# Performance work log

Hardware: AMD Instinct MI355X
Metric: run time of the kernel (lower is better)

The kernel has to match this reference:

```python
import jax, jax.numpy as jnp
import numpy as np

B, N, C, H = 2, 2048, 1024, 16
D = C // H  # head_dim = 64


def _rope_freqs(n, d_half, theta=10000.0):
    inv = 1.0 / (theta ** (np.arange(0, d_half, dtype=np.float32) / d_half))
    ang = np.arange(n, dtype=np.float32)[:, None] * inv[None, :]
    return jnp.asarray(np.cos(ang)), jnp.asarray(np.sin(ang))


def setup_inputs() -> dict:
    key = jax.random.key(0)
    ks = jax.random.split(key, 5)
    cos, sin = _rope_freqs(N, D // 2)
    s = 0.02
    return {
        "x": jax.random.normal(ks[0], (B, N, C), jnp.float32),
        "w_qkv": jax.random.normal(ks[1], (3 * C, C), jnp.float32) * s,
        "b_qkv": jnp.zeros((3 * C,), jnp.float32),
        "w_proj": jax.random.normal(ks[2], (C, C), jnp.float32) * s,
        "b_proj": jnp.zeros((C,), jnp.float32),
        "freqs_cos": cos,
        "freqs_sin": sin,
    }


def _apply_rope(t, cos, sin):
    # t: (B, H, N, D); consecutive pairs (even, odd) form complex numbers,
    # matching torch.view_as_complex on reshape(..., D//2, 2).
    te = t[..., 0::2]
    to = t[..., 1::2]
    cos = cos[None, None, :, :]  # (1,1,N,D//2)
    sin = sin[None, None, :, :]
    oe = te * cos - to * sin
    oo = te * sin + to * cos
    return jnp.stack([oe, oo], axis=-1).reshape(t.shape)


def reference(x, w_qkv, b_qkv, w_proj, b_proj, freqs_cos, freqs_sin):
    b, n, c = x.shape
    qkv = x @ w_qkv.T + b_qkv                      # (B,N,3C)
    qkv = qkv.reshape(b, n, 3, H, D).transpose(2, 0, 3, 1, 4)  # (3,B,H,N,D)
    q, k, v = qkv[0], qkv[1], qkv[2]
    q = _apply_rope(q, freqs_cos, freqs_sin)
    k = _apply_rope(k, freqs_cos, freqs_sin)
    scale = 1.0 / jnp.sqrt(jnp.asarray(D, x.dtype))
    scores = jnp.einsum("bhqd,bhkd->bhqk", q, k) * scale
    attn = jax.nn.softmax(scores, axis=-1)
    out = jnp.einsum("bhqk,bhkd->bhqd", attn, v)   # (B,H,N,D)
    out = out.transpose(0, 2, 1, 3).reshape(b, n, c)
    return out @ w_proj.T + b_proj
```

## Files before the change

kernel.cpp:

```cpp
#include <hip/hip_runtime.h>
#include <hip/hip_bf16.h>
#include <stdint.h>

#define BB 2
#define NN 2048
#define CC 1024
#define HH 16
#define DD 64
#define C3 3072

typedef __attribute__((ext_vector_type(8))) short bf16x8;
typedef __attribute__((ext_vector_type(4))) short bf16x4;
typedef __attribute__((ext_vector_type(4))) float f32x4;
typedef __attribute__((ext_vector_type(4))) unsigned short ushort4_t;

__device__ __forceinline__ unsigned short f2bf(float f) {
  union { float f; unsigned u; } v; v.f = f;
  unsigned r = v.u + 0x7FFFu + ((v.u >> 16) & 1u);
  return (unsigned short)(r >> 16);
}

#if __has_builtin(__builtin_amdgcn_exp2f)
#define EXP2(x) __builtin_amdgcn_exp2f(x)
#else
#define EXP2(x) exp2f(x)
#endif

#if __has_builtin(__builtin_amdgcn_mfma_f32_16x16x16bf16_1k)
#define HAVE_MFMA16 1
#endif

__device__ __forceinline__ unsigned pack_bf2(float a, float b) {
  union { float f; unsigned u; } ua, ub; ua.f = a; ub.f = b;
#if __has_builtin(__builtin_amdgcn_perm)
  return __builtin_amdgcn_perm(ub.u, ua.u, 0x07060302u);
#else
  return (ua.u >> 16) | (ub.u & 0xFFFF0000u);
#endif
}

#define QSCALE 0.18033688f

#define GLDS(g, l) __builtin_amdgcn_global_load_lds( \
    (const __attribute__((address_space(1))) void*)(g), \
    (__attribute__((address_space(3))) void*)(l), 16, 0, 0)

__global__ __launch_bounds__(256) void k_cvt(
    const float* __restrict__ x, const float* __restrict__ wq,
    const float* __restrict__ wp,
    unsigned short* __restrict__ xb, unsigned short* __restrict__ wqb,
    unsigned short* __restrict__ wpb)
{
  int blk = blockIdx.x;
  const float* s; unsigned short* d; int i;
  if (blk < 4096)      { s = x;  d = xb;  i = blk * 256 + threadIdx.x; }
  else if (blk < 7168) { s = wq; d = wqb; i = (blk - 4096) * 256 + threadIdx.x; }
  else                 { s = wp; d = wpb; i = (blk - 7168) * 256 + threadIdx.x; }
  float4 v = ((const float4*)s)[i];
  ushort4_t o;
  o.x = f2bf(v.x); o.y = f2bf(v.y); o.z = f2bf(v.z); o.w = f2bf(v.w);
  ((ushort4_t*)d)[i] = o;
}

__global__ __launch_bounds__(256) void k_gemm_qkv(
    const unsigned short* __restrict__ A, const unsigned short* __restrict__ Bt,
    const float* __restrict__ bias,
    const float* __restrict__ cosb, const float* __restrict__ sinb,
    unsigned short* __restrict__ Qg, unsigned short* __restrict__ Kg,
    unsigned short* __restrict__ Vt)
{
  __shared__ __align__(16) unsigned short Sh[16384];
  const int tid  = threadIdx.x;
  const int lane = tid & 63;
  const int wave = tid >> 6;
  const int bm = blockIdx.y * 128;
  const int bn = blockIdx.x * 128;
  const int wm = (wave >> 1) * 64;
  const int wn = (wave & 1) * 64;
  const int frow = lane & 15;
  const int fk   = (lane >> 4) * 8;
  const int K = 1024;
  const int NIT = K / 32;

  f32x4 acc[4][4] = {};

  const int row0 = tid >> 2, cc0 = tid & 3;
  const int row1 = row0 + 64;
  const unsigned short* Arow0 = A  + (size_t)(bm + row0) * K + cc0 * 8;
  const unsigned short* Arow1 = A  + (size_t)(bm + row1) * K + cc0 * 8;
  const unsigned short* Brow0 = Bt + (size_t)(bn + row0) * K + cc0 * 8;
  const unsigned short* Brow1 = Bt + (size_t)(bn + row1) * K + cc0 * 8;

  GLDS(Arow0, Sh + (size_t)tid * 8);
  GLDS(Brow0, Sh + 4096 + (size_t)tid * 8);
  GLDS(Arow1, Sh + (size_t)(tid + 256) * 8);
  GLDS(Brow1, Sh + 4096 + (size_t)(tid + 256) * 8);

  for (int it = 0; it < NIT; ++it) {
    const int p = it & 1;
    const unsigned short* As = Sh + p * 8192;
    const unsigned short* Bs = As + 4096;
    __syncthreads();

    if (it + 1 < NIT) {
      const int k1 = (it + 1) * 32;
      unsigned short* An = Sh + (1 - p) * 8192;
      GLDS(Arow0 + k1, An + (size_t)tid * 8);
      GLDS(Brow0 + k1, An + 4096 + (size_t)tid * 8);
      GLDS(Arow1 + k1, An + (size_t)(tid + 256) * 8);
      GLDS(Brow1 + k1, An + 4096 + (size_t)(tid + 256) * 8);
    }

    bf16x8 af[4], bfr[4];
#pragma unroll
    for (int t = 0; t < 4; ++t) {
      af[t]  = *(const bf16x8*)(As + (wm + t * 16 + frow) * 32 + fk);
      bfr[t] = *(const bf16x8*)(Bs + (wn + t * 16 + frow) * 32 + fk);
    }
#pragma unroll
    for (int mt = 0; mt < 4; ++mt)
#pragma unroll
      for (int nt = 0; nt < 4; ++nt)
        acc[mt][nt] = __builtin_amdgcn_mfma_f32_16x16x32_bf16(af[mt], bfr[nt], acc[mt][nt], 0, 0, 0);
  }
  __syncthreads();

  const int er0  = (lane >> 4) * 4;
  const int ecol = lane & 15;
  const int region = bn >> 10;
  const int gcol0 = bn + wn;
  const int h  = (gcol0 >> 6) & 15;
  const int rowg0 = bm + wm;
  const int b  = rowg0 >> 11;
  const int n0 = rowg0 & (NN - 1);
  unsigned short* wt = Sh + wave * 4096;

#pragma unroll
  for (int nt = 0; nt < 4; ++nt) {
    const int c64 = nt * 16 + ecol;
    const float bv = bias[gcol0 + c64];
    const int ii  = c64 >> 1;
#pragma unroll
    for (int mt = 0; mt < 4; ++mt)
#pragma unroll
      for (int r = 0; r < 4; ++r) {
        const int ml = mt * 16 + er0 + r;
        const int n  = n0 + ml;
        float v = acc[mt][nt][r] + bv;
        float vp = __shfl_xor(v, 1, 64);
        if (region == 2) {
          wt[c64 * 64 + ((((ml >> 3) ^ (c64 & 7)) << 3) | (ml & 7))] = f2bf(v);
        } else {
          float cth = cosb[n * 32 + ii], sth = sinb[n * 32 + ii];
          float ov = (c64 & 1) ? (vp * sth + v * cth)
                               : (v * cth - vp * sth);
          if (region == 0) ov *= QSCALE;
          wt[ml * 64 + ((((c64 >> 3) ^ (ml & 7)) << 3) | (c64 & 7))] = f2bf(ov);
        }
      }
  }

  const int rr = lane >> 3, cc = lane & 7;
  if (region == 2) {
    unsigned short* dst = Vt + (size_t)(b * HH + h) * DD * NN + n0;
#pragma unroll
    for (int it = 0; it < 8; ++it) {
      int dl = it * 8 + rr;
      bf16x8 vv = *(const bf16x8*)(wt + dl * 64 + ((cc ^ (dl & 7)) << 3));
      *(bf16x8*)(dst + (size_t)dl * NN + cc * 8) = vv;
    }
  } else {
    unsigned short* dqk = ((region == 0) ? Qg : Kg) +
                          ((size_t)(b * HH + h) * NN + n0) * DD;
#pragma unroll
    for (int it = 0; it < 8; ++it) {
      int ml = it * 8 + rr;
      bf16x8 vv = *(const bf16x8*)(wt + ml * 64 + ((cc ^ (ml & 7)) << 3));
      *(bf16x8*)(dqk + (size_t)ml * DD + cc * 8) = vv;
    }
  }
}

__global__ __launch_bounds__(256) void k_attn(
    const unsigned short* __restrict__ Qg, const unsigned short* __restrict__ Kg,
    const unsigned short* __restrict__ Vtg, unsigned short* __restrict__ Og)
{
  __shared__ __align__(16) unsigned short Ks[2][64 * 64];
  __shared__ __align__(16) unsigned short Vs[2][64 * 64];
#ifndef HAVE_MFMA16
  __shared__ __align__(16) unsigned short Ps[4][32 * 64];
#endif

  const int tid  = threadIdx.x;
  const int lane = tid & 63;
  const int wave = tid >> 6;
  const int bh = blockIdx.x >> 4;
  const int qt = blockIdx.x & 15;
  const int q0 = qt * 128 + wave * 32;
  const int frow   = lane & 15;
  const int fchunk = lane >> 4;
  const int er0  = (lane >> 4) * 4;
  const int ecol = lane & 15;

  const unsigned short* Qb = Qg  + (size_t)bh * NN * DD;
  const unsigned short* Kb = Kg  + (size_t)bh * NN * DD;
  const unsigned short* Vb = Vtg + (size_t)bh * DD * NN;

  bf16x8 qf[2][2];
#pragma unroll
  for (int m = 0; m < 2; ++m)
#pragma unroll
    for (int kt = 0; kt < 2; ++kt)
      qf[m][kt] = *(const bf16x8*)(Qb + (size_t)(q0 + m * 16 + frow) * DD + kt * 32 + fchunk * 8);

  f32x4 oacc[2][4] = {};

  const int row0 = tid >> 3, cc0 = tid & 7;
  const int sw0 = (cc0 ^ (row0 & 7)) * 8;

  GLDS(Kb + (size_t)row0 * DD + sw0,        Ks[0] + (size_t)tid * 8);
  GLDS(Vb + (size_t)row0 * NN + sw0,        Vs[0] + (size_t)tid * 8);
  GLDS(Kb + (size_t)(row0 + 32) * DD + sw0, Ks[0] + (size_t)(tid + 256) * 8);
  GLDS(Vb + (size_t)(row0 + 32) * NN + sw0, Vs[0] + (size_t)(tid + 256) * 8);

#ifdef HAVE_MFMA16
  float lsum[2] = {0.f, 0.f};

  for (int t = 0; t < NN / 64; ++t) {
    const int p = t & 1;
    __syncthreads();

    if (t + 1 < NN / 64) {
      const int j = (t + 1) * 64;
      GLDS(Kb + (size_t)(j + row0) * DD + sw0,      Ks[1 - p] + (size_t)tid * 8);
      GLDS(Vb + (size_t)row0 * NN + j + sw0,        Vs[1 - p] + (size_t)tid * 8);
      GLDS(Kb + (size_t)(j + row0 + 32) * DD + sw0, Ks[1 - p] + (size_t)(tid + 256) * 8);
      GLDS(Vb + (size_t)(row0 + 32) * NN + j + sw0, Vs[1 - p] + (size_t)(tid + 256) * 8);
    }

    f32x4 sacc[2][4] = {};
#pragma unroll
    for (int nt = 0; nt < 4; ++nt) {
      int kr = nt * 16 + frow;
      bf16x8 kf0 = *(const bf16x8*)(Ks[p] + kr * 64 + ((fchunk       ^ (kr & 7)) << 3));
      bf16x8 kf1 = *(const bf16x8*)(Ks[p] + kr * 64 + (((fchunk + 4) ^ (kr & 7)) << 3));
#pragma unroll
      for (int m = 0; m < 2; ++m) {
        sacc[m][nt] = __builtin_amdgcn_mfma_f32_16x16x32_bf16(kf0, qf[m][0], sacc[m][nt], 0, 0, 0);
        sacc[m][nt] = __builtin_amdgcn_mfma_f32_16x16x32_bf16(kf1, qf[m][1], sacc[m][nt], 0, 0, 0);
      }
    }

    bf16x4 pfr[2][4];
#pragma unroll
    for (int m = 0; m < 2; ++m)
#pragma unroll
      for (int nt = 0; nt < 4; ++nt) {
        float e0 = EXP2(sacc[m][nt][0]);
        float e1 = EXP2(sacc[m][nt][1]);
        float e2 = EXP2(sacc[m][nt][2]);
        float e3 = EXP2(sacc[m][nt][3]);
        lsum[m] += (e0 + e1) + (e2 + e3);
        union { unsigned u[2]; bf16x4 v; } pk;
        pk.u[0] = pack_bf2(e0, e1);
        pk.u[1] = pack_bf2(e2, e3);
        pfr[m][nt] = pk.v;
      }

#pragma unroll
    for (int dt = 0; dt < 4; ++dt) {
      int vr = dt * 16 + frow;
      bf16x4 vfr[4];
#pragma unroll
      for (int c = 0; c < 4; ++c)
        vfr[c] = *(const bf16x4*)(Vs[p] + vr * 64 +
                   (((2 * c + (fchunk >> 1)) ^ (vr & 7)) << 3) + (fchunk & 1) * 4);
#pragma unroll
      for (int m = 0; m < 2; ++m)
#pragma unroll
        for (int c = 0; c < 4; ++c)
          oacc[m][dt] = __builtin_amdgcn_mfma_f32_16x16x16bf16_1k(pfr[m][c], vfr[c], oacc[m][dt], 0, 0, 0);
    }
  }

  const int b = bh >> 4;
  const int h = bh & 15;
#pragma unroll
  for (int m = 0; m < 2; ++m) {
    lsum[m] += __shfl_xor(lsum[m], 16, 64);
    lsum[m] += __shfl_xor(lsum[m], 32, 64);
    float linv[4];
#pragma unroll
    for (int r = 0; r < 4; ++r)
      linv[r] = 1.0f / __shfl(lsum[m], er0 + r, 64);
#pragma unroll
    for (int dt = 0; dt < 4; ++dt)
#pragma unroll
      for (int r = 0; r < 4; ++r) {
        int qrow = q0 + m * 16 + er0 + r;
        int d = dt * 16 + ecol;
        Og[(size_t)(b * NN + qrow) * CC + h * DD + d] = f2bf(oacc[m][dt][r] * linv[r]);
      }
  }

#else
  bf16x8 ones;
#pragma unroll
  for (int i = 0; i < 8; ++i) ones[i] = (short)0x3F80;
  f32x4 lacc[2] = {};

  for (int t = 0; t < NN / 64; ++t) {
    const int p = t & 1;
    __syncthreads();
    if (t + 1 < NN / 64) {
      const int j = (t + 1) * 64;
      GLDS(Kb + (size_t)(j + row0) * DD + sw0,      Ks[1 - p] + (size_t)tid * 8);
      GLDS(Vb + (size_t)row0 * NN + j + sw0,        Vs[1 - p] + (size_t)tid * 8);
      GLDS(Kb + (size_t)(j + row0 + 32) * DD + sw0, Ks[1 - p] + (size_t)(tid + 256) * 8);
      GLDS(Vb + (size_t)(row0 + 32) * NN + j + sw0, Vs[1 - p] + (size_t)(tid + 256) * 8);
    }
    f32x4 sacc[2][4] = {};
#pragma unroll
    for (int nt = 0; nt < 4; ++nt) {
      int kr = nt * 16 + frow;
      bf16x8 kf0 = *(const bf16x8*)(Ks[p] + kr * 64 + ((fchunk       ^ (kr & 7)) << 3));
      bf16x8 kf1 = *(const bf16x8*)(Ks[p] + kr * 64 + (((fchunk + 4) ^ (kr & 7)) << 3));
#pragma unroll
      for (int m = 0; m < 2; ++m) {
        sacc[m][nt] = __builtin_amdgcn_mfma_f32_16x16x32_bf16(qf[m][0], kf0, sacc[m][nt], 0, 0, 0);
        sacc[m][nt] = __builtin_amdgcn_mfma_f32_16x16x32_bf16(qf[m][1], kf1, sacc[m][nt], 0, 0, 0);
      }
    }
#pragma unroll
    for (int m = 0; m < 2; ++m)
#pragma unroll
      for (int r = 0; r < 4; ++r) {
        int prow = m * 16 + er0 + r;
#pragma unroll
        for (int nt = 0; nt < 4; ++nt) {
          float pv = EXP2(sacc[m][nt][r]);
          union { float f; unsigned u; } cv; cv.f = pv;
          int col = nt * 16 + ecol;
          Ps[wave][prow * 64 + (((col >> 3) ^ (prow & 7)) << 3) + (col & 7)] =
              (unsigned short)(cv.u >> 16);
        }
      }
    bf16x8 pf0[2], pf1[2];
#pragma unroll
    for (int m = 0; m < 2; ++m) {
      int pr = m * 16 + frow;
      pf0[m] = *(const bf16x8*)(&Ps[wave][pr * 64 + ((fchunk       ^ (pr & 7)) << 3)]);
      pf1[m] = *(const bf16x8*)(&Ps[wave][pr * 64 + (((fchunk + 4) ^ (pr & 7)) << 3)]);
      lacc[m] = __builtin_amdgcn_mfma_f32_16x16x32_bf16(pf0[m], ones, lacc[m], 0, 0, 0);
      lacc[m] = __builtin_amdgcn_mfma_f32_16x16x32_bf16(pf1[m], ones, lacc[m], 0, 0, 0);
    }
#pragma unroll
    for (int dt = 0; dt < 4; ++dt) {
      int vr = dt * 16 + frow;
      bf16x8 vf0 = *(const bf16x8*)(Vs[p] + vr * 64 + ((fchunk       ^ (vr & 7)) << 3));
      bf16x8 vf1 = *(const bf16x8*)(Vs[p] + vr * 64 + (((fchunk + 4) ^ (vr & 7)) << 3));
#pragma unroll
      for (int m = 0; m < 2; ++m) {
        oacc[m][dt] = __builtin_amdgcn_mfma_f32_16x16x32_bf16(pf0[m], vf0, oacc[m][dt], 0, 0, 0);
        oacc[m][dt] = __builtin_amdgcn_mfma_f32_16x16x32_bf16(pf1[m], vf1, oacc[m][dt], 0, 0, 0);
      }
    }
  }
  const int b = bh >> 4;
  const int h = bh & 15;
#pragma unroll
  for (int m = 0; m < 2; ++m)
#pragma unroll
    for (int dt = 0; dt < 4; ++dt)
#pragma unroll
      for (int r = 0; r < 4; ++r) {
        int qrow = q0 + m * 16 + er0 + r;
        int d = dt * 16 + ecol;
        Og[(size_t)(b * NN + qrow) * CC + h * DD + d] = f2bf(oacc[m][dt][r] / lacc[m][r]);
      }
#endif
}

__global__ __launch_bounds__(256) void k_gemm_proj(
    const unsigned short* __restrict__ A, const unsigned short* __restrict__ Bt,
    const float* __restrict__ bias, float* __restrict__ Co)
{
  __shared__ __align__(16) unsigned short As[2][64 * 32];
  __shared__ __align__(16) unsigned short Bs[2][128 * 32];
  const int tid  = threadIdx.x;
  const int lane = tid & 63;
  const int wave = tid >> 6;
  const int bm = blockIdx.y * 64;
  const int bn = blockIdx.x * 128;
  const int wm = (wave >> 1) * 32;
  const int wn = (wave & 1) * 64;
  const int frow = lane & 15;
  const int fk   = (lane >> 4) * 8;
  const int K = 1024;
  const int NIT = K / 32;

  f32x4 acc[2][4] = {};

  const int row0 = tid >> 2, cc0 = tid & 3;
  const unsigned short* Arow  = A  + (size_t)(bm + row0) * K + cc0 * 8;
  const unsigned short* Brow0 = Bt + (size_t)(bn + row0) * K + cc0 * 8;
  const unsigned short* Brow1 = Bt + (size_t)(bn + row0 + 64) * K + cc0 * 8;

  GLDS(Arow,  As[0] + (size_t)tid * 8);
  GLDS(Brow0, Bs[0] + (size_t)tid * 8);
  GLDS(Brow1, Bs[0] + (size_t)(tid + 256) * 8);

  for (int it = 0; it < NIT; ++it) {
    const int p = it & 1;
    __syncthreads();

    if (it + 1 < NIT) {
      const int k1 = (it + 1) * 32;
      GLDS(Arow  + k1, As[1 - p] + (size_t)tid * 8);
      GLDS(Brow0 + k1, Bs[1 - p] + (size_t)tid * 8);
      GLDS(Brow1 + k1, Bs[1 - p] + (size_t)(tid + 256) * 8);
    }

    bf16x8 af[2], bfr[4];
#pragma unroll
    for (int t = 0; t < 2; ++t)
      af[t] = *(const bf16x8*)(As[p] + (wm + t * 16 + frow) * 32 + fk);
#pragma unroll
    for (int t = 0; t < 4; ++t)
      bfr[t] = *(const bf16x8*)(Bs[p] + (wn + t * 16 + frow) * 32 + fk);
#pragma unroll
    for (int mt = 0; mt < 2; ++mt)
#pragma unroll
      for (int nt = 0; nt < 4; ++nt)
        acc[mt][nt] = __builtin_amdgcn_mfma_f32_16x16x32_bf16(af[mt], bfr[nt], acc[mt][nt], 0, 0, 0);
  }

  const int er0  = (lane >> 4) * 4;
  const int ecol = lane & 15;
#pragma unroll
  for (int nt = 0; nt < 4; ++nt) {
    int col = bn + wn + nt * 16 + ecol;
    float bv = bias[col];
#pragma unroll
    for (int mt = 0; mt < 2; ++mt)
#pragma unroll
      for (int r = 0; r < 4; ++r) {
        int rowg = bm + wm + mt * 16 + er0 + r;
        Co[(size_t)rowg * CC + col] = acc[mt][nt][r] + bv;
      }
  }
}

extern "C" void kernel_launch(void* const* d_in, const int* in_sizes, int n_in,
                              void* d_out, int out_size, void* d_ws, size_t ws_size,
                              hipStream_t stream)
{
  const float* x      = (const float*)d_in[0];
  const float* w_qkv  = (const float*)d_in[1];
  const float* b_qkv  = (const float*)d_in[2];
  const float* w_proj = (const float*)d_in[3];
  const float* b_proj = (const float*)d_in[4];
  const float* fcos   = (const float*)d_in[5];
  const float* fsin   = (const float*)d_in[6];
  float* out = (float*)d_out;

  char* ws = (char*)d_ws;
  unsigned short* xb     = (unsigned short*)(ws);
  unsigned short* wqkvb  = (unsigned short*)(ws + 8388608);
  unsigned short* wprojb = (unsigned short*)(ws + 14680064);
  unsigned short* Qb     = (unsigned short*)(ws + 16777216);
  unsigned short* Kb     = (unsigned short*)(ws + 25165824);
  unsigned short* Vtb    = (unsigned short*)(ws + 33554432);
  unsigned short* aob    = (unsigned short*)(ws + 41943040);

  k_cvt<<<8192, 256, 0, stream>>>(x, w_qkv, w_proj, xb, wqkvb, wprojb);

  k_gemm_qkv<<<dim3(24, 32), 256, 0, stream>>>(xb, wqkvb, b_qkv, fcos, fsin,
                                               Qb, Kb, Vtb);

  k_attn<<<512, 256, 0, stream>>>(Qb, Kb, Vtb, aob);

  k_gemm_proj<<<dim3(8, 64), 256, 0, stream>>>(aob, wprojb, b_proj, out);
}
```

Before: 215.5 us.

## Switch attention kernel to 32x32x16 MFMA tiles with transposed score layout

Rewrites the attention inner loop to use 32x32x16 bf16 MFMA for both QK^T and PV instead of 16x16 variants, computing transposed scores so the exponentiated probabilities feed the PV MFMA directly from registers. LDS offsets are precomputed per lane, and the row sum reduces across two half-waves only. This aims to cut MFMA instruction count and LDS fragment loads per tile, at the cost of larger accumulator register footprint and a different output write pattern. The non-MFMA16 fallback path is removed.

```diff
diff --git a/kernel.cpp b/kernel.cpp
--- a/kernel.cpp
+++ b/kernel.cpp
@@ -12,6 +12,7 @@
 typedef __attribute__((ext_vector_type(8))) short bf16x8;
 typedef __attribute__((ext_vector_type(4))) short bf16x4;
 typedef __attribute__((ext_vector_type(4))) float f32x4;
+typedef __attribute__((ext_vector_type(16))) float f32x16;
 typedef __attribute__((ext_vector_type(4))) unsigned short ushort4_t;
 
 __device__ __forceinline__ unsigned short f2bf(float f) {
@@ -24,10 +25,6 @@
 #define EXP2(x) __builtin_amdgcn_exp2f(x)
 #else
 #define EXP2(x) exp2f(x)
-#endif
-
-#if __has_builtin(__builtin_amdgcn_mfma_f32_16x16x16bf16_1k)
-#define HAVE_MFMA16 1
 #endif
 
 __device__ __forceinline__ unsigned pack_bf2(float a, float b) {
@@ -187,9 +184,6 @@
 {
   __shared__ __align__(16) unsigned short Ks[2][64 * 64];
   __shared__ __align__(16) unsigned short Vs[2][64 * 64];
-#ifndef HAVE_MFMA16
-  __shared__ __align__(16) unsigned short Ps[4][32 * 64];
-#endif
 
   const int tid  = threadIdx.x;
   const int lane = tid & 63;
@@ -197,23 +191,31 @@
   const int bh = blockIdx.x >> 4;
   const int qt = blockIdx.x & 15;
   const int q0 = qt * 128 + wave * 32;
-  const int frow   = lane & 15;
-  const int fchunk = lane >> 4;
-  const int er0  = (lane >> 4) * 4;
-  const int ecol = lane & 15;
+  const int l31 = lane & 31;
+  const int hi  = lane >> 5;
+  const int s7  = l31 & 7;
 
   const unsigned short* Qb = Qg  + (size_t)bh * NN * DD;
   const unsigned short* Kb = Kg  + (size_t)bh * NN * DD;
   const unsigned short* Vb = Vtg + (size_t)bh * DD * NN;
 
-  bf16x8 qf[2][2];
-#pragma unroll
-  for (int m = 0; m < 2; ++m)
-#pragma unroll
-    for (int kt = 0; kt < 2; ++kt)
-      qf[m][kt] = *(const bf16x8*)(Qb + (size_t)(q0 + m * 16 + frow) * DD + kt * 32 + fchunk * 8);
-
-  f32x4 oacc[2][4] = {};
+  int koff[4];
+#pragma unroll
+  for (int x = 0; x < 4; ++x)
+    koff[x] = l31 * 64 + (((2 * x + hi) ^ s7) << 3);
+
+  int vkoff[8];
+#pragma unroll
+  for (int c = 0; c < 8; ++c)
+    vkoff[c] = l31 * 64 + ((c ^ s7) << 3) + hi * 4;
+
+  bf16x8 qf[4];
+#pragma unroll
+  for (int dc = 0; dc < 4; ++dc)
+    qf[dc] = *(const bf16x8*)(Qb + (size_t)(q0 + l31) * DD + dc * 16 + hi * 8);
+
+  f32x16 oacc[2] = {};
+  float lsum = 0.f;
 
   const int row0 = tid >> 3, cc0 = tid & 7;
   const int sw0 = (cc0 ^ (row0 & 7)) * 8;
@@ -223,11 +225,10 @@
   GLDS(Kb + (size_t)(row0 + 32) * DD + sw0, Ks[0] + (size_t)(tid + 256) * 8);
   GLDS(Vb + (size_t)(row0 + 32) * NN + sw0, Vs[0] + (size_t)(tid + 256) * 8);
 
-#ifdef HAVE_MFMA16
-  float lsum[2] = {0.f, 0.f};
-
   for (int t = 0; t < NN / 64; ++t) {
     const int p = t & 1;
+    const unsigned short* Kp = Ks[p];
+    const unsigned short* Vp = Vs[p];
     __syncthreads();
 
     if (t + 1 < NN / 64) {
@@ -238,147 +239,52 @@
       GLDS(Vb + (size_t)(row0 + 32) * NN + j + sw0, Vs[1 - p] + (size_t)(tid + 256) * 8);
     }
 
-    f32x4 sacc[2][4] = {};
-#pragma unroll
-    for (int nt = 0; nt < 4; ++nt) {
-      int kr = nt * 16 + frow;
-      bf16x8 kf0 = *(const bf16x8*)(Ks[p] + kr * 64 + ((fchunk       ^ (kr & 7)) << 3));
-      bf16x8 kf1 = *(const bf16x8*)(Ks[p] + kr * 64 + (((fchunk + 4) ^ (kr & 7)) << 3));
-#pragma unroll
-      for (int m = 0; m < 2; ++m) {
-        sacc[m][nt] = __builtin_amdgcn_mfma_f32_16x16x32_bf16(kf0, qf[m][0], sacc[m][nt], 0, 0, 0);
-        sacc[m][nt] = __builtin_amdgcn_mfma_f32_16x16x32_bf16(kf1, qf[m][1], sacc[m][nt], 0, 0, 0);
-      }
-    }
-
-    bf16x4 pfr[2][4];
-#pragma unroll
-    for (int m = 0; m < 2; ++m)
-#pragma unroll
-      for (int nt = 0; nt < 4; ++nt) {
-        float e0 = EXP2(sacc[m][nt][0]);
-        float e1 = EXP2(sacc[m][nt][1]);
-        float e2 = EXP2(sacc[m][nt][2]);
-        float e3 = EXP2(sacc[m][nt][3]);
-        lsum[m] += (e0 + e1) + (e2 + e3);
-        union { unsigned u[2]; bf16x4 v; } pk;
-        pk.u[0] = pack_bf2(e0, e1);
-        pk.u[1] = pack_bf2(e2, e3);
-        pfr[m][nt] = pk.v;
-      }
-
-#pragma unroll
-    for (int dt = 0; dt < 4; ++dt) {
-      int vr = dt * 16 + frow;
-      bf16x4 vfr[4];
-#pragma unroll
-      for (int c = 0; c < 4; ++c)
-        vfr[c] = *(const bf16x4*)(Vs[p] + vr * 64 +
-                   (((2 * c + (fchunk >> 1)) ^ (vr & 7)) << 3) + (fchunk & 1) * 4);
-#pragma unroll
-      for (int m = 0; m < 2; ++m)
-#pragma unroll
-        for (int c = 0; c < 4; ++c)
-          oacc[m][dt] = __builtin_amdgcn_mfma_f32_16x16x16bf16_1k(pfr[m][c], vfr[c], oacc[m][dt], 0, 0, 0);
-    }
-  }
-
+    f32x16 sacc[2] = {};
+#pragma unroll
+    for (int T = 0; T < 2; ++T)
+#pragma unroll
+      for (int dc = 0; dc < 4; ++dc) {
+        bf16x8 kf = *(const bf16x8*)(Kp + T * 2048 + koff[dc]);
+        sacc[T] = __builtin_amdgcn_mfma_f32_32x32x16_bf16(kf, qf[dc], sacc[T], 0, 0, 0);
+      }
+
+#pragma unroll
+    for (int T = 0; T < 2; ++T) {
+      unsigned pk[8];
+#pragma unroll
+      for (int jj = 0; jj < 8; ++jj) {
+        float e0 = EXP2(sacc[T][2 * jj]);
+        float e1 = EXP2(sacc[T][2 * jj + 1]);
+        lsum += e0 + e1;
+        pk[jj] = pack_bf2(e0, e1);
+      }
+      union { unsigned u[4]; bf16x8 v; } fa, fb;
+      fa.u[0] = pk[0]; fa.u[1] = pk[1]; fa.u[2] = pk[2]; fa.u[3] = pk[3];
+      fb.u[0] = pk[4]; fb.u[1] = pk[5]; fb.u[2] = pk[6]; fb.u[3] = pk[7];
+#pragma unroll
+      for (int dt = 0; dt < 2; ++dt) {
+        union { bf16x4 h[2]; bf16x8 w; } v0, v1;
+        v0.h[0] = *(const bf16x4*)(Vp + dt * 2048 + vkoff[4 * T + 0]);
+        v0.h[1] = *(const bf16x4*)(Vp + dt * 2048 + vkoff[4 * T + 1]);
+        v1.h[0] = *(const bf16x4*)(Vp + dt * 2048 + vkoff[4 * T + 2]);
+        v1.h[1] = *(const bf16x4*)(Vp + dt * 2048 + vkoff[4 * T + 3]);
+        oacc[dt] = __builtin_amdgcn_mfma_f32_32x32x16_bf16(fa.v, v0.w, oacc[dt], 0, 0, 0);
+        oacc[dt] = __builtin_amdgcn_mfma_f32_32x32x16_bf16(fb.v, v1.w, oacc[dt], 0, 0, 0);
+      }
+    }
+  }
+
+  float ltot = lsum + __shfl_xor(lsum, 32, 64);
   const int b = bh >> 4;
   const int h = bh & 15;
 #pragma unroll
-  for (int m = 0; m < 2; ++m) {
-    lsum[m] += __shfl_xor(lsum[m], 16, 64);
-    lsum[m] += __shfl_xor(lsum[m], 32, 64);
-    float linv[4];
-#pragma unroll
-    for (int r = 0; r < 4; ++r)
-      linv[r] = 1.0f / __shfl(lsum[m], er0 + r, 64);
-#pragma unroll
-    for (int dt = 0; dt < 4; ++dt)
-#pragma unroll
-      for (int r = 0; r < 4; ++r) {
-        int qrow = q0 + m * 16 + er0 + r;
-        int d = dt * 16 + ecol;
-        Og[(size_t)(b * NN + qrow) * CC + h * DD + d] = f2bf(oacc[m][dt][r] * linv[r]);
-      }
-  }
-
-#else
-  bf16x8 ones;
-#pragma unroll
-  for (int i = 0; i < 8; ++i) ones[i] = (short)0x3F80;
-  f32x4 lacc[2] = {};
-
-  for (int t = 0; t < NN / 64; ++t) {
-    const int p = t & 1;
-    __syncthreads();
-    if (t + 1 < NN / 64) {
-      const int j = (t + 1) * 64;
-      GLDS(Kb + (size_t)(j + row0) * DD + sw0,      Ks[1 - p] + (size_t)tid * 8);
-      GLDS(Vb + (size_t)row0 * NN + j + sw0,        Vs[1 - p] + (size_t)tid * 8);
-      GLDS(Kb + (size_t)(j + row0 + 32) * DD + sw0, Ks[1 - p] + (size_t)(tid + 256) * 8);
-      GLDS(Vb + (size_t)(row0 + 32) * NN + j + sw0, Vs[1 - p] + (size_t)(tid + 256) * 8);
-    }
-    f32x4 sacc[2][4] = {};
-#pragma unroll
-    for (int nt = 0; nt < 4; ++nt) {
-      int kr = nt * 16 + frow;
-      bf16x8 kf0 = *(const bf16x8*)(Ks[p] + kr * 64 + ((fchunk       ^ (kr & 7)) << 3));
-      bf16x8 kf1 = *(const bf16x8*)(Ks[p] + kr * 64 + (((fchunk + 4) ^ (kr & 7)) << 3));
-#pragma unroll
-      for (int m = 0; m < 2; ++m) {
-        sacc[m][nt] = __builtin_amdgcn_mfma_f32_16x16x32_bf16(qf[m][0], kf0, sacc[m][nt], 0, 0, 0);
-        sacc[m][nt] = __builtin_amdgcn_mfma_f32_16x16x32_bf16(qf[m][1], kf1, sacc[m][nt], 0, 0, 0);
-      }
-    }
-#pragma unroll
-    for (int m = 0; m < 2; ++m)
-#pragma unroll
-      for (int r = 0; r < 4; ++r) {
-        int prow = m * 16 + er0 + r;
-#pragma unroll
-        for (int nt = 0; nt < 4; ++nt) {
-          float pv = EXP2(sacc[m][nt][r]);
-          union { float f; unsigned u; } cv; cv.f = pv;
-          int col = nt * 16 + ecol;
-          Ps[wave][prow * 64 + (((col >> 3) ^ (prow & 7)) << 3) + (col & 7)] =
-              (unsigned short)(cv.u >> 16);
-        }
-      }
-    bf16x8 pf0[2], pf1[2];
-#pragma unroll
-    for (int m = 0; m < 2; ++m) {
-      int pr = m * 16 + frow;
-      pf0[m] = *(const bf16x8*)(&Ps[wave][pr * 64 + ((fchunk       ^ (pr & 7)) << 3)]);
-      pf1[m] = *(const bf16x8*)(&Ps[wave][pr * 64 + (((fchunk + 4) ^ (pr & 7)) << 3)]);
-      lacc[m] = __builtin_amdgcn_mfma_f32_16x16x32_bf16(pf0[m], ones, lacc[m], 0, 0, 0);
-      lacc[m] = __builtin_amdgcn_mfma_f32_16x16x32_bf16(pf1[m], ones, lacc[m], 0, 0, 0);
-    }
-#pragma unroll
-    for (int dt = 0; dt < 4; ++dt) {
-      int vr = dt * 16 + frow;
-      bf16x8 vf0 = *(const bf16x8*)(Vs[p] + vr * 64 + ((fchunk       ^ (vr & 7)) << 3));
-      bf16x8 vf1 = *(const bf16x8*)(Vs[p] + vr * 64 + (((fchunk + 4) ^ (vr & 7)) << 3));
-#pragma unroll
-      for (int m = 0; m < 2; ++m) {
-        oacc[m][dt] = __builtin_amdgcn_mfma_f32_16x16x32_bf16(pf0[m], vf0, oacc[m][dt], 0, 0, 0);
-        oacc[m][dt] = __builtin_amdgcn_mfma_f32_16x16x32_bf16(pf1[m], vf1, oacc[m][dt], 0, 0, 0);
-      }
-    }
-  }
-  const int b = bh >> 4;
-  const int h = bh & 15;
-#pragma unroll
-  for (int m = 0; m < 2; ++m)
-#pragma unroll
-    for (int dt = 0; dt < 4; ++dt)
-#pragma unroll
-      for (int r = 0; r < 4; ++r) {
-        int qrow = q0 + m * 16 + er0 + r;
-        int d = dt * 16 + ecol;
-        Og[(size_t)(b * NN + qrow) * CC + h * DD + d] = f2bf(oacc[m][dt][r] / lacc[m][r]);
-      }
-#endif
+  for (int r = 0; r < 16; ++r) {
+    const int qr = (r & 3) + 8 * (r >> 2) + 4 * hi;
+    const float linv = 1.0f / __shfl(ltot, qr, 64);
+    unsigned short* orow = Og + (size_t)(b * NN + q0 + qr) * CC + h * DD + l31;
+    orow[0]  = f2bf(oacc[0][r] * linv);
+    orow[32] = f2bf(oacc[1][r] * linv);
+  }
 }
 
 __global__ __launch_bounds__(256) void k_gemm_proj(
```

Result: faster. 202.5 us (-6.1%).
